# Optimization experiments

Hardware: AMD Instinct MI355X
Metric: run time of the kernel (lower is better)

## Reference

```python
import math
import jax, jax.numpy as jnp
import numpy as np

N, C, H, W = 32, 128, 56, 56


def unfold3(x, axis, dil):
    """F.unfold with 3-tap kernel along `axis`, dilation `dil`, padding `dil`.
    Input (n,c,h,w) -> output (n,c,3,h,w); tap k takes offset (k-1)*dil."""
    pad_cfg = [(0, 0)] * 4
    pad_cfg[axis] = (dil, dil)
    xp = jnp.pad(x, pad_cfg)
    size = x.shape[axis]
    taps = [jax.lax.slice_in_dim(xp, k * dil, k * dil + size, axis=axis) for k in range(3)]
    return jnp.stack(taps, axis=2)


def setup_inputs() -> dict:
    key = jax.random.key(0)
    k0, k1, k2, k3, k4 = jax.random.split(key, 5)
    x = jax.random.normal(k0, (N, C, H, W), dtype=jnp.float32)
    # trunc_normal_(std=0.02) approximated by normal * 0.02
    p2 = jax.random.normal(k1, (1, 1, 3, 1, W), dtype=jnp.float32) * 0.02
    # 1x1 conv weight (out=C, in=3C), kaiming-ish scale
    p3 = jax.random.normal(k2, (C, 3 * C), dtype=jnp.float32) * (1.0 / math.sqrt(3 * C))
    p5 = jax.random.normal(k3, (1, 1, H, W), dtype=jnp.float32) * 0.02
    p10 = jax.random.normal(k4, (1, C, 3, H, W), dtype=jnp.float32) * 0.02
    return {"x": x, "p2": p2, "p3": p3, "p5": p5, "p10": p10}


def reference(x, p2, p3, p5, p10):
    n, c, h, w = x.shape
    # t_1: vertical 3-tap unfold, dilation 2 -> (n,c,3,h,w)
    t1 = unfold3(x, axis=2, dil=2)
    t2 = p2 * t1                                              # (n,c,3,h,w)
    # t_3: 1x1 conv over the c*3 channel view
    t3 = jnp.einsum('nkhw,ck->nchw', t1.reshape(n, c * 3, h, w), p3)
    # t_4: horizontal 3-tap unfold, dilation 1
    t4 = unfold3(t3, axis=3, dil=1)                           # (n,c,3,h,w)
    t5 = p5 * t3                                              # (n,c,h,w)
    # t_7/t_8: horizontal 3-tap unfold of x, dilation 2, softmax over taps
    t7 = unfold3(x, axis=3, dil=2)
    t8 = jax.nn.softmax(t7, axis=2)                           # (n,c,3,h,w)
    # t_9: bmm over spatial dim -> (n,c,c*3)
    t9 = jnp.einsum('ncx,ndx->ncd', x.reshape(n, c, h * w),
                    t4.reshape(n, c * 3, h * w)) / math.sqrt(h * w)
    t10 = p10 * t8                                            # (n,c,3,h,w)
    # t_11: memory-reinterpreting view: (n,1,c,h,w) - (n,3,c,h,w) -> back to (n,c,3,h,w)
    t11 = (t5[:, None] - t2.reshape(n, 3, c, h, w)).reshape(n, c, 3, h, w)
    t12 = t11 - t10                                           # (n,c,3,h,w)
    # t_13: bmm over c*3 -> (n,c,h*w)
    t13 = jnp.einsum('ncd,ndx->ncx', t9,
                     t12.reshape(n, c * 3, h * w)) / math.sqrt(c * 3)
    return t13.reshape(n, c, h, w)
```

## Files before the change

### kernel.cpp

```cpp
#include <hip/hip_runtime.h>
#include <stdint.h>

#define NB 32
#define C_ 128
#define H_ 56
#define W_ 56
#define HW 3136
#define KD 384

typedef __attribute__((ext_vector_type(8))) short bf16x8;
typedef __attribute__((ext_vector_type(4))) float f32x4;

__device__ inline uint16_t f2bf(float f) {
    uint32_t u = __float_as_uint(f);
    return (uint16_t)((u + 0x7FFFu + ((u >> 16) & 1u)) >> 16);
}
__device__ inline float bf2f(uint16_t b) {
    return __uint_as_float(((uint32_t)b) << 16);
}

__global__ __launch_bounds__(256) void p1_xtp(const float* __restrict__ x,
                                              uint16_t* __restrict__ xtp) {
    __shared__ uint16_t lt[56][136];
    const int h = blockIdx.x, n = blockIdx.y, tid = threadIdx.x;
    const int c = tid >> 1, wh = tid & 1;
    const float* xr = &x[(((size_t)n * C_ + c) * H_ + h) * W_ + wh * 28];
#pragma unroll
    for (int q = 0; q < 7; ++q) {
        float4 v = *(const float4*)&xr[q * 4];
        int wb = wh * 28 + q * 4;
        lt[wb + 0][c] = f2bf(v.x);
        lt[wb + 1][c] = f2bf(v.y);
        lt[wb + 2][c] = f2bf(v.z);
        lt[wb + 3][c] = f2bf(v.w);
    }
    __syncthreads();
    const int w = tid >> 2, qc = tid & 3;
    uint16_t* dst = &xtp[((((size_t)n * H_ + h) * 64 + w)) * C_ + qc * 32];
    if (w < 56) {
        const uint32_t* s = (const uint32_t*)&lt[w][qc * 32];
        uint4 a = *(const uint4*)(s);
        uint4 b = *(const uint4*)(s + 4);
        uint4 c4 = *(const uint4*)(s + 8);
        uint4 d4 = *(const uint4*)(s + 12);
        *(uint4*)dst = a;
        *(uint4*)(dst + 8) = b;
        *(uint4*)(dst + 16) = c4;
        *(uint4*)(dst + 24) = d4;
    } else {
        uint4 z = {0, 0, 0, 0};
        *(uint4*)dst = z;
        *(uint4*)(dst + 8) = z;
        *(uint4*)(dst + 16) = z;
        *(uint4*)(dst + 24) = z;
    }
}

__global__ __launch_bounds__(256) void p2_ap(const float* __restrict__ p3,
                                             uint16_t* __restrict__ ap) {
    int i = blockIdx.x * 256 + threadIdx.x;
    int c = i / KD, dp = i - c * KD;
    int tap = dp >> 7, c2 = dp & 127;
    ap[i] = f2bf(p3[c * KD + 3 * c2 + tap]);
}

__global__ __launch_bounds__(256) void k1(const uint16_t* __restrict__ xtp,
                                          const uint16_t* __restrict__ ap,
                                          uint16_t* __restrict__ t3b) {
    __shared__ uint16_t smem[3 * 64 * 128];
    const int h = blockIdx.x, n = blockIdx.y, tid = threadIdx.x;
    const int lane = tid & 63, wid = tid >> 6;
    const int wm = wid >> 1, wn = wid & 1;

    for (int t = tid; t < 3072; t += 256) {
        int tap = t >> 10, r = t & 1023, w = r >> 4, qp = r & 15;
        int q = qp ^ (w & 7);
        int hh = h + 2 * (tap - 1);
        uint4 v = {0, 0, 0, 0};
        if ((unsigned)hh < (unsigned)H_)
            v = *(const uint4*)&xtp[((((size_t)n * H_ + hh) * 64 + w)) * C_ + q * 8];
        *(uint4*)&smem[tap * 8192 + w * 128 + qp * 8] = v;
    }
    __syncthreads();

    f32x4 acc[4][2] = {};
    for (int ks = 0; ks < 12; ++ks) {
        int tap = ks >> 2, kk = ks & 3;
        bf16x8 a[4], b[2];
#pragma unroll
        for (int m = 0; m < 4; ++m) {
            int c = wm * 64 + m * 16 + (lane & 15);
            a[m] = *(const bf16x8*)&ap[c * KD + ks * 32 + (lane >> 4) * 8];
        }
#pragma unroll
        for (int nt = 0; nt < 2; ++nt) {
            int w = wn * 32 + nt * 16 + (lane & 15);
            int q = kk * 4 + (lane >> 4);
            b[nt] = *(const bf16x8*)&smem[tap * 8192 + w * 128 + (q ^ (w & 7)) * 8];
        }
#pragma unroll
        for (int m = 0; m < 4; ++m)
#pragma unroll
            for (int nt = 0; nt < 2; ++nt)
                acc[m][nt] = __builtin_amdgcn_mfma_f32_16x16x32_bf16(a[m], b[nt], acc[m][nt], 0, 0, 0);
    }
    __syncthreads();

    uint16_t* lrow = smem;
#pragma unroll
    for (int m = 0; m < 4; ++m)
#pragma unroll
        for (int nt = 0; nt < 2; ++nt)
#pragma unroll
            for (int r = 0; r < 4; ++r) {
                int c = wm * 64 + m * 16 + (lane >> 4) * 4 + r;
                int w = wn * 32 + nt * 16 + (lane & 15);
                lrow[c * 72 + w] = f2bf(acc[m][nt][r]);
            }
    __syncthreads();

    const uint32_t* lrowd = (const uint32_t*)smem;
    for (int t = tid; t < 1024; t += 256) {
        int c = t >> 3, ch = t & 7;
        int m0 = c * 36 + ch * 4;
        uint4 o = make_uint4(lrowd[m0], lrowd[m0 + 1], lrowd[m0 + 2], lrowd[m0 + 3]);
        *(uint4*)&t3b[(((size_t)n * C_ + c) * H_ + h) * 64 + ch * 8] = o;
    }
}

__global__ __launch_bounds__(512) void k2(const float* __restrict__ x,
                                          const uint16_t* __restrict__ t3b,
                                          float* __restrict__ part) {
    __shared__ uint16_t xs[128 * 64];
    __shared__ uint16_t ts[128 * 64];
    const int bx = blockIdx.x;
    const int hc = bx / 3, tap = bx - hc * 3;
    const int n = blockIdx.y;
    const int tid = threadIdx.x, lane = tid & 63, wid = tid >> 6;
    const int wm = wid >> 2, wn = wid & 3;

    f32x4 acc[4][2] = {};
    for (int hr = 0; hr < 8; ++hr) {
        const int h = hc * 8 + hr;
        __syncthreads();
        for (int t = tid; t < 1024; t += 512) {
            int c = t >> 3, qp = t & 7, q = qp ^ (c & 7);
            uint4 v = {0, 0, 0, 0};
            if (q < 7) {
                const float* s = &x[(((size_t)n * C_ + c) * H_ + h) * W_ + q * 8];
                float4 f0 = *(const float4*)s, f1 = *(const float4*)(s + 4);
                v.x = (uint32_t)f2bf(f0.x) | ((uint32_t)f2bf(f0.y) << 16);
                v.y = (uint32_t)f2bf(f0.z) | ((uint32_t)f2bf(f0.w) << 16);
                v.z = (uint32_t)f2bf(f1.x) | ((uint32_t)f2bf(f1.y) << 16);
                v.w = (uint32_t)f2bf(f1.z) | ((uint32_t)f2bf(f1.w) << 16);
            }
            *(uint4*)&xs[c * 64 + qp * 8] = v;
        }
        for (int t = tid; t < 1024; t += 512) {
            int c2 = t >> 3, qp = t & 7, q = qp ^ (c2 & 7);
            const uint16_t* row = &t3b[(((size_t)n * C_ + c2) * H_ + h) * 64];
            uint4 v = *(const uint4*)&row[q * 8];
            uint4 o;
            if (tap == 1) {
                o = v;
            } else if (tap == 2) {
                uint32_t nx = (q < 7) ? *(const uint32_t*)&row[q * 8 + 8] : 0u;
                o.x = (v.y << 16) | (v.x >> 16);
                o.y = (v.z << 16) | (v.y >> 16);
                o.z = (v.w << 16) | (v.z >> 16);
                o.w = (nx << 16)  | (v.w >> 16);
            } else {
                uint32_t pv = (q > 0) ? *(const uint32_t*)&row[q * 8 - 2] : 0u;
                o.x = (v.x << 16) | (pv >> 16);
                o.y = (v.y << 16) | (v.x >> 16);
                o.z = (v.z << 16) | (v.y >> 16);
                o.w = (v.w << 16) | (v.z >> 16);
            }
            *(uint4*)&ts[c2 * 64 + qp * 8] = o;
        }
        __syncthreads();
#pragma unroll
        for (int ks = 0; ks < 2; ++ks) {
            bf16x8 a[4], b[2];
#pragma unroll
            for (int m = 0; m < 4; ++m) {
                int c = wm * 64 + m * 16 + (lane & 15);
                int q = ks * 4 + (lane >> 4);
                a[m] = *(const bf16x8*)&xs[c * 64 + (q ^ (c & 7)) * 8];
            }
#pragma unroll
            for (int nt = 0; nt < 2; ++nt) {
                int c2 = wn * 32 + nt * 16 + (lane & 15);
                int q = ks * 4 + (lane >> 4);
                b[nt] = *(const bf16x8*)&ts[c2 * 64 + (q ^ (c2 & 7)) * 8];
            }
#pragma unroll
            for (int m = 0; m < 4; ++m)
#pragma unroll
                for (int nt = 0; nt < 2; ++nt)
                    acc[m][nt] = __builtin_amdgcn_mfma_f32_16x16x32_bf16(a[m], b[nt], acc[m][nt], 0, 0, 0);
        }
    }
#pragma unroll
    for (int m = 0; m < 4; ++m)
#pragma unroll
        for (int nt = 0; nt < 2; ++nt)
#pragma unroll
            for (int r = 0; r < 4; ++r) {
                int c = wm * 64 + m * 16 + (lane >> 4) * 4 + r;
                int col = wn * 32 + nt * 16 + (lane & 15);
                part[((((size_t)bx * NB + n) * C_ + c) << 7) + col] = acc[m][nt][r];
            }
}

__global__ __launch_bounds__(256) void kr(const float* __restrict__ part,
                                          uint16_t* __restrict__ acat) {
    int idx = blockIdx.x * 256 + threadIdx.x;
    int fl = idx * 4;
    int nc = fl / KD, dp = fl - nc * KD;
    int tap = dp >> 7, c2 = dp & 127;
    float4 s = make_float4(0.f, 0.f, 0.f, 0.f);
#pragma unroll
    for (int hc = 0; hc < 7; ++hc) {
        const float4 v = *(const float4*)&part[((((size_t)(hc * 3 + tap)) * NB * C_ + nc) << 7) + c2];
        s.x += v.x; s.y += v.y; s.z += v.z; s.w += v.w;
    }
    const float sc = 1.f / 56.f;
    uint2 o;
    o.x = (uint32_t)f2bf(s.x * sc) | ((uint32_t)f2bf(s.y * sc) << 16);
    o.y = (uint32_t)f2bf(s.z * sc) | ((uint32_t)f2bf(s.w * sc) << 16);
    *(uint2*)&acat[(size_t)nc * 512 + dp] = o;
}

__global__ __launch_bounds__(256) void ka2(uint16_t* __restrict__ acat) {
    int t = blockIdx.x * 256 + threadIdx.x;
    int nc = t >> 3, m0 = (t & 7) * 16;
    uint16_t* row = &acat[(size_t)nc * 512];
#pragma unroll
    for (int mi = 0; mi < 16; ++mi) {
        int m = m0 + mi;
        float s = 0.f;
#pragma unroll
        for (int r = 0; r < 3; ++r) {
            int d = m + 128 * r;
            int q3 = d / 3;
            int dp = (d - q3 * 3) * 128 + q3;
            s += bf2f(row[dp]);
        }
        row[384 + m] = f2bf(s);
    }
}

__global__ __launch_bounds__(256) void kt(const float* __restrict__ p10,
                                          uint16_t* __restrict__ p10t) {
    const int h = blockIdx.x, tid = threadIdx.x;
    for (int idx = tid; idx < 3072; idx += 256) {
        int w = idx & 63, ch = idx >> 6;
        int dp0 = ch * 8;
        uint32_t pk[4];
#pragma unroll
        for (int j = 0; j < 8; ++j) {
            int dp = dp0 + j;
            int tap = dp >> 7, c2 = dp & 127;
            int dor = 3 * c2 + tap;
            float v = (w < W_) ? p10[(size_t)dor * HW + h * W_ + w] : 0.f;
            uint16_t bb = f2bf(v);
            if (j & 1) pk[j >> 1] |= ((uint32_t)bb) << 16;
            else       pk[j >> 1] = bb;
        }
        *(uint4*)&p10t[((size_t)h * 64 + w) * KD + dp0] = *(const uint4*)pk;
    }
}

__global__ __launch_bounds__(256) void k3(const uint16_t* __restrict__ xtp,
                                          const uint16_t* __restrict__ t3b,
                                          const uint16_t* __restrict__ acat,
                                          const uint16_t* __restrict__ p10t,
                                          const float* __restrict__ p2,
                                          const float* __restrict__ p5,
                                          float* __restrict__ out) {
    __shared__ uint16_t tsm[64 * 512];
    const int h = blockIdx.x, n = blockIdx.y, tid = threadIdx.x;
    const int lane = tid & 63, wid = tid >> 6;
    const int w = lane;
    const int wsw = w & 7;
    float p2v[3];
#pragma unroll
    for (int tap = 0; tap < 3; ++tap)
        p2v[tap] = (w < W_) ? p2[tap * W_ + w] : 0.f;

    const size_t xrow = ((size_t)n * H_ + h) * 64;
    const int wm2 = (w >= 2) ? w - 2 : 0;
    const int wp2 = (w + 2 < 64) ? w + 2 : 63;

#pragma unroll
    for (int cc = 0; cc < 4; ++cc) {
        const int c2b = (wid * 4 + cc) * 8;
        bf16x8 xh_v = *(const bf16x8*)&xtp[(xrow + w) * C_ + c2b];
        bf16x8 xm_v = *(const bf16x8*)&xtp[(xrow + wm2) * C_ + c2b];
        bf16x8 xp_v = *(const bf16x8*)&xtp[(xrow + wp2) * C_ + c2b];
        float sm[3][8];
#pragma unroll
        for (int j = 0; j < 8; ++j) {
            float a1 = bf2f((uint16_t)xh_v[j]);
            float a0 = (w >= 2) ? bf2f((uint16_t)xm_v[j]) : 0.f;
            float a2 = bf2f((uint16_t)xp_v[j]);
            float mx = fmaxf(a0, fmaxf(a1, a2));
            float e0 = __expf(a0 - mx), e1 = __expf(a1 - mx), e2 = __expf(a2 - mx);
            float rs = 1.f / (e0 + e1 + e2);
            sm[0][j] = e0 * rs; sm[1][j] = e1 * rs; sm[2][j] = e2 * rs;
        }
#pragma unroll
        for (int tap = 0; tap < 3; ++tap) {
            bf16x8 xhh;
            float p2e;
            if (tap == 1) { xhh = xh_v; p2e = p2v[1]; }
            else {
                const int hh = h + 2 * (tap - 1);
                const bool hok = (unsigned)hh < (unsigned)H_;
                const int hhc = hok ? hh : h;
                xhh = *(const bf16x8*)&xtp[(((size_t)n * H_ + hhc) * 64 + w) * C_ + c2b];
                p2e = hok ? p2v[tap] : 0.f;
            }
            bf16x8 pv = *(const bf16x8*)&p10t[((size_t)h * 64 + w) * KD + tap * 128 + c2b];
            uint32_t pk[4];
#pragma unroll
            for (int j = 0; j < 8; ++j) {
                float val = -(p2e * bf2f((uint16_t)xhh[j]) + bf2f((uint16_t)pv[j]) * sm[tap][j]);
                uint16_t bb = f2bf(val);
                if (j & 1) pk[j >> 1] |= ((uint32_t)bb) << 16;
                else       pk[j >> 1] = bb;
            }
            int q = tap * 16 + (c2b >> 3);
            *(uint4*)&tsm[w * 512 + ((q ^ wsw) << 3)] = *(const uint4*)pk;
        }
    }

    {
        const int c2f = tid >> 1;
        const int whf = (tid & 1) << 5;
        const uint16_t* t3r = &t3b[(((size_t)n * C_ + c2f) * H_ + h) * 64 + whf];
        const int qf = 48 + (c2f >> 3);
        const int cf7 = c2f & 7;
#pragma unroll
        for (int g = 0; g < 4; ++g) {
            bf16x8 tv = *(const bf16x8*)&t3r[g * 8];
#pragma unroll
            for (int j = 0; j < 8; ++j) {
                int ww = whf + g * 8 + j;
                float p5v = (ww < W_) ? p5[h * W_ + ww] : 0.f;
                tsm[ww * 512 + ((qf ^ (ww & 7)) << 3) + cf7] = f2bf(p5v * bf2f((uint16_t)tv[j]));
            }
        }
    }
    __syncthreads();

    const int wm = wid >> 1, wn = wid & 1;
    f32x4 acc[4][2] = {};
    for (int ks = 0; ks < 16; ++ks) {
        bf16x8 a[4], b[2];
#pragma unroll
        for (int m = 0; m < 4; ++m) {
            int c = wm * 64 + m * 16 + (lane & 15);
            a[m] = *(const bf16x8*)&acat[((size_t)n * C_ + c) * 512 + ks * 32 + (lane >> 4) * 8];
        }
#pragma unroll
        for (int nt = 0; nt < 2; ++nt) {
            int ww = wn * 32 + nt * 16 + (lane & 15);
            int q = ks * 4 + (lane >> 4);
            b[nt] = *(const bf16x8*)&tsm[ww * 512 + ((q ^ (ww & 7)) << 3)];
        }
#pragma unroll
        for (int m = 0; m < 4; ++m)
#pragma unroll
            for (int nt = 0; nt < 2; ++nt)
                acc[m][nt] = __builtin_amdgcn_mfma_f32_16x16x32_bf16(a[m], b[nt], acc[m][nt], 0, 0, 0);
    }

    const float s = 0.05103103630798287f;
#pragma unroll
    for (int m = 0; m < 4; ++m)
#pragma unroll
        for (int nt = 0; nt < 2; ++nt) {
            int ww = wn * 32 + nt * 16 + (lane & 15);
            if (ww < W_) {
                int c = wm * 64 + m * 16 + (lane >> 4) * 4;
                float* dst = &out[(((size_t)n * C_ + c) * H_ + h) * W_ + ww];
#pragma unroll
                for (int r = 0; r < 4; ++r) dst[(size_t)r * HW] = acc[m][nt][r] * s;
            }
        }
}

extern "C" void kernel_launch(void* const* d_in, const int* in_sizes, int n_in,
                              void* d_out, int out_size, void* d_ws, size_t ws_size,
                              hipStream_t stream) {
    const float* x   = (const float*)d_in[0];
    const float* p2  = (const float*)d_in[1];
    const float* p3  = (const float*)d_in[2];
    const float* p5  = (const float*)d_in[3];
    const float* p10 = (const float*)d_in[4];
    float* out = (float*)d_out;

    uint8_t* w8 = (uint8_t*)d_ws;
    uint16_t* t3b  = (uint16_t*)(w8);
    uint16_t* ap   = (uint16_t*)(w8 + 29360128);
    uint16_t* xtp  = (uint16_t*)(w8 + 29458432);
    float*    part = (float*)   (w8 + 58818560);
    uint16_t* p10t = (uint16_t*)(w8 + 58818560);
    uint16_t* acat = (uint16_t*)(w8 + 102858752);

    p1_xtp<<<dim3(H_, NB), 256, 0, stream>>>(x, xtp);
    p2_ap<<<dim3(192), 256, 0, stream>>>(p3, ap);
    k1<<<dim3(H_, NB), 256, 0, stream>>>(xtp, ap, t3b);
    k2<<<dim3(21, NB), 512, 0, stream>>>(x, t3b, part);
    kr<<<dim3(1536), 256, 0, stream>>>(part, acat);
    ka2<<<dim3(128), 256, 0, stream>>>(acat);
    kt<<<dim3(H_), 256, 0, stream>>>(p10, p10t);
    k3<<<dim3(H_, NB), 256, 0, stream>>>(xtp, t3b, acat, p10t, p2, p5, out);
}
```

Baseline: 262.0 us.

## Split k3 blocks across half-width rows to raise occupancy

The final GEMM kernel now gives each block 32 columns of one row instead of all 64, which doubles the grid to 112×32 and halves the shared-memory tile to 32KB. Per-thread work is remapped: each warp owns 32 output channels across 32 columns, and a launch-bounds occupancy hint of 4 is added. The aim is more resident blocks and better latency hiding. The cost is that each block still reads the full A (acat) rows for its batch, so A traffic doubles.

```diff
diff --git a/kernel.cpp b/kernel.cpp
--- a/kernel.cpp
+++ b/kernel.cpp
@@ -272,106 +272,111 @@
     }
 }
 
-__global__ __launch_bounds__(256) void k3(const uint16_t* __restrict__ xtp,
-                                          const uint16_t* __restrict__ t3b,
-                                          const uint16_t* __restrict__ acat,
-                                          const uint16_t* __restrict__ p10t,
-                                          const float* __restrict__ p2,
-                                          const float* __restrict__ p5,
-                                          float* __restrict__ out) {
-    __shared__ uint16_t tsm[64 * 512];
-    const int h = blockIdx.x, n = blockIdx.y, tid = threadIdx.x;
+__global__ __launch_bounds__(256, 4) void k3(const uint16_t* __restrict__ xtp,
+                                             const uint16_t* __restrict__ t3b,
+                                             const uint16_t* __restrict__ acat,
+                                             const uint16_t* __restrict__ p10t,
+                                             const float* __restrict__ p2,
+                                             const float* __restrict__ p5,
+                                             float* __restrict__ out) {
+    __shared__ uint16_t tsm[32 * 512];
+    const int bx = blockIdx.x, n = blockIdx.y, tid = threadIdx.x;
+    const int h = bx >> 1, wbase = (bx & 1) << 5;
     const int lane = tid & 63, wid = tid >> 6;
-    const int w = lane;
-    const int wsw = w & 7;
-    float p2v[3];
-#pragma unroll
-    for (int tap = 0; tap < 3; ++tap)
-        p2v[tap] = (w < W_) ? p2[tap * W_ + w] : 0.f;
-
-    const size_t xrow = ((size_t)n * H_ + h) * 64;
-    const int wm2 = (w >= 2) ? w - 2 : 0;
-    const int wp2 = (w + 2 < 64) ? w + 2 : 63;
-
-#pragma unroll
-    for (int cc = 0; cc < 4; ++cc) {
-        const int c2b = (wid * 4 + cc) * 8;
-        bf16x8 xh_v = *(const bf16x8*)&xtp[(xrow + w) * C_ + c2b];
-        bf16x8 xm_v = *(const bf16x8*)&xtp[(xrow + wm2) * C_ + c2b];
-        bf16x8 xp_v = *(const bf16x8*)&xtp[(xrow + wp2) * C_ + c2b];
-        float sm[3][8];
-#pragma unroll
-        for (int j = 0; j < 8; ++j) {
-            float a1 = bf2f((uint16_t)xh_v[j]);
-            float a0 = (w >= 2) ? bf2f((uint16_t)xm_v[j]) : 0.f;
-            float a2 = bf2f((uint16_t)xp_v[j]);
-            float mx = fmaxf(a0, fmaxf(a1, a2));
-            float e0 = __expf(a0 - mx), e1 = __expf(a1 - mx), e2 = __expf(a2 - mx);
-            float rs = 1.f / (e0 + e1 + e2);
-            sm[0][j] = e0 * rs; sm[1][j] = e1 * rs; sm[2][j] = e2 * rs;
-        }
-#pragma unroll
-        for (int tap = 0; tap < 3; ++tap) {
-            bf16x8 xhh;
-            float p2e;
-            if (tap == 1) { xhh = xh_v; p2e = p2v[1]; }
-            else {
-                const int hh = h + 2 * (tap - 1);
-                const bool hok = (unsigned)hh < (unsigned)H_;
-                const int hhc = hok ? hh : h;
-                xhh = *(const bf16x8*)&xtp[(((size_t)n * H_ + hhc) * 64 + w) * C_ + c2b];
-                p2e = hok ? p2v[tap] : 0.f;
-            }
-            bf16x8 pv = *(const bf16x8*)&p10t[((size_t)h * 64 + w) * KD + tap * 128 + c2b];
-            uint32_t pk[4];
+
+    {
+        const int w = tid & 31, seg = tid >> 5;
+        const int wg = wbase + w;
+        const int wsw = w & 7;
+        float p2v[3];
+#pragma unroll
+        for (int tap = 0; tap < 3; ++tap)
+            p2v[tap] = (wg < W_) ? p2[tap * W_ + wg] : 0.f;
+        const size_t xrow = ((size_t)n * H_ + h) * 64;
+        const int wgm2 = (wg >= 2) ? wg - 2 : 0;
+        const int wgp2 = (wg + 2 < 64) ? wg + 2 : 63;
+
+#pragma unroll
+        for (int s = 0; s < 2; ++s) {
+            const int c2b = (seg + s * 8) * 8;
+            bf16x8 xh_v = *(const bf16x8*)&xtp[(xrow + wg) * C_ + c2b];
+            bf16x8 xm_v = *(const bf16x8*)&xtp[(xrow + wgm2) * C_ + c2b];
+            bf16x8 xp_v = *(const bf16x8*)&xtp[(xrow + wgp2) * C_ + c2b];
+            float sm[3][8];
 #pragma unroll
             for (int j = 0; j < 8; ++j) {
-                float val = -(p2e * bf2f((uint16_t)xhh[j]) + bf2f((uint16_t)pv[j]) * sm[tap][j]);
-                uint16_t bb = f2bf(val);
-                if (j & 1) pk[j >> 1] |= ((uint32_t)bb) << 16;
-                else       pk[j >> 1] = bb;
-            }
-            int q = tap * 16 + (c2b >> 3);
-            *(uint4*)&tsm[w * 512 + ((q ^ wsw) << 3)] = *(const uint4*)pk;
+                float a1 = bf2f((uint16_t)xh_v[j]);
+                float a0 = (wg >= 2) ? bf2f((uint16_t)xm_v[j]) : 0.f;
+                float a2 = bf2f((uint16_t)xp_v[j]);
+                float mx = fmaxf(a0, fmaxf(a1, a2));
+                float e0 = __expf(a0 - mx), e1 = __expf(a1 - mx), e2 = __expf(a2 - mx);
+                float rs = 1.f / (e0 + e1 + e2);
+                sm[0][j] = e0 * rs; sm[1][j] = e1 * rs; sm[2][j] = e2 * rs;
+            }
+#pragma unroll
+            for (int tap = 0; tap < 3; ++tap) {
+                bf16x8 xhh;
+                float p2e;
+                if (tap == 1) { xhh = xh_v; p2e = p2v[1]; }
+                else {
+                    const int hh = h + 2 * (tap - 1);
+                    const bool hok = (unsigned)hh < (unsigned)H_;
+                    const int hhc = hok ? hh : h;
+                    xhh = *(const bf16x8*)&xtp[(((size_t)n * H_ + hhc) * 64 + wg) * C_ + c2b];
+                    p2e = hok ? p2v[tap] : 0.f;
+                }
+                bf16x8 pv = *(const bf16x8*)&p10t[((size_t)h * 64 + wg) * KD + tap * 128 + c2b];
+                uint32_t pk[4];
+#pragma unroll
+                for (int j = 0; j < 8; ++j) {
+                    float val = -(p2e * bf2f((uint16_t)xhh[j]) + bf2f((uint16_t)pv[j]) * sm[tap][j]);
+                    uint16_t bb = f2bf(val);
+                    if (j & 1) pk[j >> 1] |= ((uint32_t)bb) << 16;
+                    else       pk[j >> 1] = bb;
+                }
+                int q = (tap * 128 + c2b) >> 3;
+                *(uint4*)&tsm[w * 512 + ((q ^ wsw) << 3)] = *(const uint4*)pk;
+            }
         }
     }
 
     {
         const int c2f = tid >> 1;
-        const int whf = (tid & 1) << 5;
-        const uint16_t* t3r = &t3b[(((size_t)n * C_ + c2f) * H_ + h) * 64 + whf];
+        const int whl = (tid & 1) << 4;
+        const uint16_t* t3r = &t3b[(((size_t)n * C_ + c2f) * H_ + h) * 64 + wbase + whl];
         const int qf = 48 + (c2f >> 3);
         const int cf7 = c2f & 7;
 #pragma unroll
-        for (int g = 0; g < 4; ++g) {
+        for (int g = 0; g < 2; ++g) {
             bf16x8 tv = *(const bf16x8*)&t3r[g * 8];
 #pragma unroll
             for (int j = 0; j < 8; ++j) {
-                int ww = whf + g * 8 + j;
-                float p5v = (ww < W_) ? p5[h * W_ + ww] : 0.f;
-                tsm[ww * 512 + ((qf ^ (ww & 7)) << 3) + cf7] = f2bf(p5v * bf2f((uint16_t)tv[j]));
+                int wl = whl + g * 8 + j;
+                int wwg = wbase + wl;
+                float p5v = (wwg < W_) ? p5[h * W_ + wwg] : 0.f;
+                tsm[wl * 512 + ((qf ^ (wl & 7)) << 3) + cf7] = f2bf(p5v * bf2f((uint16_t)tv[j]));
             }
         }
     }
     __syncthreads();
 
-    const int wm = wid >> 1, wn = wid & 1;
-    f32x4 acc[4][2] = {};
+    const int wm = wid;
+    f32x4 acc[2][2] = {};
     for (int ks = 0; ks < 16; ++ks) {
-        bf16x8 a[4], b[2];
-#pragma unroll
-        for (int m = 0; m < 4; ++m) {
-            int c = wm * 64 + m * 16 + (lane & 15);
+        bf16x8 a[2], b[2];
+#pragma unroll
+        for (int m = 0; m < 2; ++m) {
+            int c = wm * 32 + m * 16 + (lane & 15);
             a[m] = *(const bf16x8*)&acat[((size_t)n * C_ + c) * 512 + ks * 32 + (lane >> 4) * 8];
         }
 #pragma unroll
         for (int nt = 0; nt < 2; ++nt) {
-            int ww = wn * 32 + nt * 16 + (lane & 15);
+            int wl = nt * 16 + (lane & 15);
             int q = ks * 4 + (lane >> 4);
-            b[nt] = *(const bf16x8*)&tsm[ww * 512 + ((q ^ (ww & 7)) << 3)];
-        }
-#pragma unroll
-        for (int m = 0; m < 4; ++m)
+            b[nt] = *(const bf16x8*)&tsm[wl * 512 + ((q ^ (wl & 7)) << 3)];
+        }
+#pragma unroll
+        for (int m = 0; m < 2; ++m)
 #pragma unroll
             for (int nt = 0; nt < 2; ++nt)
                 acc[m][nt] = __builtin_amdgcn_mfma_f32_16x16x32_bf16(a[m], b[nt], acc[m][nt], 0, 0, 0);
@@ -379,13 +384,13 @@
 
     const float s = 0.05103103630798287f;
 #pragma unroll
-    for (int m = 0; m < 4; ++m)
+    for (int m = 0; m < 2; ++m)
 #pragma unroll
         for (int nt = 0; nt < 2; ++nt) {
-            int ww = wn * 32 + nt * 16 + (lane & 15);
-            if (ww < W_) {
-                int c = wm * 64 + m * 16 + (lane >> 4) * 4;
-                float* dst = &out[(((size_t)n * C_ + c) * H_ + h) * W_ + ww];
+            int wwg = wbase + nt * 16 + (lane & 15);
+            if (wwg < W_) {
+                int c = wm * 32 + m * 16 + (lane >> 4) * 4;
+                float* dst = &out[(((size_t)n * C_ + c) * H_ + h) * W_ + wwg];
 #pragma unroll
                 for (int r = 0; r < 4; ++r) dst[(size_t)r * HW] = acc[m][nt][r] * s;
             }
@@ -417,5 +422,5 @@
     kr<<<dim3(1536), 256, 0, stream>>>(part, acat);
     ka2<<<dim3(128), 256, 0, stream>>>(acat);
     kt<<<dim3(H_), 256, 0, stream>>>(p10, p10t);
-    k3<<<dim3(H_, NB), 256, 0, stream>>>(xtp, t3b, acat, p10t, p2, p5, out);
-}
+    k3<<<dim3(112, NB), 256, 0, stream>>>(xtp, t3b, acat, p10t, p2, p5, out);
+}
```

New measurement: 249.1 us. -4.9%, faster.
